# Kernel optimization log

Hardware: AMD Instinct MI355X
Metric: run time of the kernel (lower is better)

The kernel has to match this reference:

```python
import jax, jax.numpy as jnp
import numpy as np

B, DIM, H, W = 8, 512, 32, 32
HC, WC = 32, 32
NH, DH = 8, 64
DE = NH * DH  # dim_embed = 512


def setup_inputs() -> dict:
    key = jax.random.key(0)
    ks = jax.random.split(key, 6)
    return {
        "x": jax.random.normal(ks[0], (B, DIM, H, W), jnp.float32),
        "context": jax.random.normal(ks[1], (B, DIM, HC, WC), jnp.float32),
        "gamma": jnp.ones((DIM, 1, 1), jnp.float32),
        "w_q": jax.random.normal(ks[2], (DE, DIM), jnp.float32) * 0.02,
        "w_k": jax.random.normal(ks[3], (DE, DIM), jnp.float32) * 0.02,
        "w_v": jax.random.normal(ks[4], (DE, DIM), jnp.float32) * 0.02,
        "w_proj": jax.random.normal(ks[5], (DIM, DE), jnp.float32) * 0.02,
    }


def _rms_norm(t, gamma, scale):
    # torch F.normalize(dim=1): x / max(||x||_2, 1e-12) along channel axis
    nrm = jnp.sqrt(jnp.sum(t * t, axis=1, keepdims=True))
    return t / jnp.maximum(nrm, 1e-12) * scale * gamma


def _split_heads(t, h, w):
    # 'b (c n) h w -> (b n) (h w) c' with c=DH, n=NH
    b = t.shape[0]
    t = t.reshape(b, DH, NH, h, w).transpose(0, 2, 3, 4, 1)  # b n h w c
    return t.reshape(b * NH, h * w, DH)


def reference(x, context, gamma, w_q, w_k, w_v, w_proj):
    scale = float(DIM) ** 0.5
    xn = _rms_norm(x, gamma, scale)
    # faithful to source bug: self.norm (not norm_context) applied to context
    cn = _rms_norm(context, gamma, scale)

    q = jnp.einsum('bchw,oc->bohw', xn, w_q)
    k = jnp.einsum('bchw,oc->bohw', cn, w_k)
    v = jnp.einsum('bchw,oc->bohw', cn, w_v)

    q = _split_heads(q, H, W)      # (B*NH, H*W, DH)
    k = _split_heads(k, HC, WC)    # (B*NH, HC*WC, DH)
    v = _split_heads(v, HC, WC)

    qk = jnp.einsum('bmc,bnc->bmn', q, k) * (float(DH) ** -0.5)
    attn = jnp.einsum('bmn,bnc->bmc', jax.nn.softmax(qk, axis=-1) + 1e-8, v) + 1e-8

    # '(b n) (h w) c -> b (c n) h w'
    attn = attn.reshape(B, NH, H, W, DH).transpose(0, 4, 1, 2, 3).reshape(B, DE, H, W)
    return jnp.einsum('bchw,oc->bohw', attn, w_proj)
```

## Files before the change

kernel.cpp:

```cpp
#include <hip/hip_runtime.h>
#include <hip/hip_bf16.h>


typedef _Float16 half8v __attribute__((ext_vector_type(8)));
typedef __attribute__((ext_vector_type(4))) float float4v;

__device__ inline ushort f2h(float f) {
  union { _Float16 h; ushort u; } cv;
  cv.h = (_Float16)f;
  return cv.u;
}

__device__ inline void stage16(const void* g, void* l) {
  __builtin_amdgcn_global_load_lds(
      (const __attribute__((address_space(1))) unsigned*)g,
      (__attribute__((address_space(3))) unsigned*)l, 16, 0, 0);
}

__global__ __launch_bounds__(256) void tq_kernel(
    const float* __restrict__ x, const float* __restrict__ ctx,
    ushort* __restrict__ xT, ushort* __restrict__ cT,
    float* __restrict__ sx, float* __restrict__ sc) {
  const int tensor = blockIdx.z;
  const int b = blockIdx.y;
  const int pos0 = blockIdx.x << 5;
  const float* src = tensor ? ctx : x;
  ushort* dstT = tensor ? cT : xT;
  float* dstS = tensor ? sc : sx;
  const int t = threadIdx.x;

  __shared__ ushort tile[32 * 512];
  __shared__ float part[32][32];
  unsigned* tile32 = (unsigned*)tile;

  const int pcq = t & 7;
  const int crg = t >> 3;
  float ssq[4] = {0.f, 0.f, 0.f, 0.f};

  const float* srcb = src + ((size_t)b * 512) * 1024 + pos0;
  for (int p = 0; p < 8; ++p) {
    const int cr0 = p * 64 + crg * 2;
    float4 v0 = *(const float4*)&srcb[(size_t)cr0 * 1024 + pcq * 4];
    float4 v1 = *(const float4*)&srcb[(size_t)(cr0 + 1) * 1024 + pcq * 4];
    ssq[0] += v0.x * v0.x + v1.x * v1.x;
    ssq[1] += v0.y * v0.y + v1.y * v1.y;
    ssq[2] += v0.z * v0.z + v1.z * v1.z;
    ssq[3] += v0.w * v0.w + v1.w * v1.w;
    const int cp = cr0 >> 1;
    float e0[4] = {v0.x, v0.y, v0.z, v0.w};
    float e1[4] = {v1.x, v1.y, v1.z, v1.w};
#pragma unroll
    for (int j = 0; j < 4; ++j) {
      const int posl = pcq * 4 + j;
      unsigned pk = (unsigned)f2h(e0[j]) | ((unsigned)f2h(e1[j]) << 16);
      tile32[posl * 256 + (cp ^ posl)] = pk;
    }
  }
#pragma unroll
  for (int j = 0; j < 4; ++j) part[crg][pcq * 4 + j] = ssq[j];
  __syncthreads();
  if (t < 32) {
    float s = 0.f;
#pragma unroll
    for (int g2 = 0; g2 < 32; ++g2) s += part[g2][t];
    dstS[b * 1024 + pos0 + t] = 22.627416997969522f / fmaxf(sqrtf(s), 1e-12f);
  }
  ushort* ob = dstT + ((size_t)b * 1024 + pos0) * 512;
#pragma unroll
  for (int ii = 0; ii < 8; ++ii) {
    const int m = t + ii * 256;
    const int posl = m >> 6, c16 = m & 63;
    uint4 u;
    u.x = tile32[posl * 256 + ((c16 * 4 + 0) ^ posl)];
    u.y = tile32[posl * 256 + ((c16 * 4 + 1) ^ posl)];
    u.z = tile32[posl * 256 + ((c16 * 4 + 2) ^ posl)];
    u.w = tile32[posl * 256 + ((c16 * 4 + 3) ^ posl)];
    *(uint4*)&ob[(size_t)posl * 512 + c16 * 8] = u;
  }
}

__global__ __launch_bounds__(256) void wconv_kernel(
    const float* __restrict__ wq, const float* __restrict__ wk,
    const float* __restrict__ wv, const float* __restrict__ wp,
    const float* __restrict__ gamma, ushort* __restrict__ wf) {
  const int m = blockIdx.y;
  const float* W = (m == 0) ? wq : (m == 1) ? wk : (m == 2) ? wv : wp;
  const int r = blockIdx.x * 4 + (threadIdx.x >> 6);
  const int c8 = (threadIdx.x & 63) * 8;
  ushort h[8];
  if (m < 3) {
    const int o = ((r & 63) << 3) + (r >> 6);
    const float* wr_ = &W[(size_t)o * 512 + c8];
#pragma unroll
    for (int j = 0; j < 8; ++j) h[j] = f2h(wr_[j] * gamma[c8 + j]);
  } else {
#pragma unroll
    for (int j = 0; j < 8; ++j) {
      const int cc = c8 + j;
      const int cs = ((cc & 63) << 3) + (cc >> 6);
      h[j] = f2h(W[(size_t)r * 512 + cs]);
    }
  }
  ushort* dst = &wf[((size_t)m * 512 + r) * 512 + c8];
  uint4 u;
  u.x = (unsigned)h[0] | ((unsigned)h[1] << 16);
  u.y = (unsigned)h[2] | ((unsigned)h[3] << 16);
  u.z = (unsigned)h[4] | ((unsigned)h[5] << 16);
  u.w = (unsigned)h[6] | ((unsigned)h[7] << 16);
  *(uint4*)dst = u;
}

__global__ __launch_bounds__(256, 2) void qkv_kernel(
    const ushort* __restrict__ xT, const ushort* __restrict__ cT,
    const ushort* __restrict__ wf, const float* __restrict__ sx,
    const float* __restrict__ sc, ushort* __restrict__ qh,
    ushort* __restrict__ kh, ushort* __restrict__ vt) {
  const int z = blockIdx.z;
  const int proj = z % 3;
  const int b = z / 3;
  const ushort* XT = (proj == 0) ? xT : cT;
  const float* S = (proj == 0) ? sx : sc;
  const ushort* WF = wf + (size_t)proj * 262144;
  const int pos0 = blockIdx.x << 7;
  const int o0 = blockIdx.y << 7;

  __shared__ __align__(16) unsigned char lds[65536];
  unsigned char* Al = lds;
  unsigned char* Bl = lds + 32768;

  const int t = threadIdx.x, w = t >> 6, lane = t & 63;
  const int g = lane >> 4, l15 = lane & 15;
  const int wr = w >> 1, wc = w & 1;
  const int srow_ = lane >> 3;
  const int sslot16 = ((lane & 7) ^ srow_) << 4;

  const unsigned char* Asrc =
      (const unsigned char*)(XT + ((size_t)b * 1024 + pos0) * 512);
  const unsigned char* Bsrc = (const unsigned char*)(WF + (size_t)o0 * 512);

#define QSTAGE(buf, kk)                                                     \
  do {                                                                      \
    _Pragma("unroll") for (int i = 0; i < 4; ++i) {                         \
      const int j = (w << 2) + i;                                           \
      stage16(Asrc + (size_t)((j << 3) + srow_) * 1024 + (kk)*128 + sslot16,\
              Al + (buf)*16384 + (j << 10));                                \
      stage16(Bsrc + (size_t)((j << 3) + srow_) * 1024 + (kk)*128 + sslot16,\
              Bl + (buf)*16384 + (j << 10));                                \
    }                                                                       \
  } while (0)

  float4v acc[4][4];
#pragma unroll
  for (int i = 0; i < 4; ++i)
#pragma unroll
    for (int j2 = 0; j2 < 4; ++j2) acc[i][j2] = (float4v){0.f, 0.f, 0.f, 0.f};

  QSTAGE(0, 0);
  __syncthreads();

  for (int kk = 0; kk < 8; ++kk) {
    const int cur = kk & 1;
    if (kk < 7) QSTAGE(cur ^ 1, kk + 1);
    const unsigned char* At = Al + cur * 16384;
    const unsigned char* Bt = Bl + cur * 16384;
    half8v af[4][2], bf[4][2];
#pragma unroll
    for (int mt = 0; mt < 4; ++mt) {
      const int row = (wr << 6) + (mt << 4) + l15;
      const unsigned char* rb = At + row * 128;
      af[mt][0] = *(const half8v*)(rb + (((g) ^ (row & 7)) << 4));
      af[mt][1] = *(const half8v*)(rb + (((4 + g) ^ (row & 7)) << 4));
    }
#pragma unroll
    for (int nt = 0; nt < 4; ++nt) {
      const int row = (wc << 6) + (nt << 4) + l15;
      const unsigned char* rb = Bt + row * 128;
      bf[nt][0] = *(const half8v*)(rb + (((g) ^ (row & 7)) << 4));
      bf[nt][1] = *(const half8v*)(rb + (((4 + g) ^ (row & 7)) << 4));
    }
    if (proj < 2) {
#pragma unroll
      for (int mt = 0; mt < 4; ++mt)
#pragma unroll
        for (int nt = 0; nt < 4; ++nt) {
          acc[mt][nt] = __builtin_amdgcn_mfma_f32_16x16x32_f16(
              af[mt][0], bf[nt][0], acc[mt][nt], 0, 0, 0);
          acc[mt][nt] = __builtin_amdgcn_mfma_f32_16x16x32_f16(
              af[mt][1], bf[nt][1], acc[mt][nt], 0, 0, 0);
        }
    } else {
#pragma unroll
      for (int mt = 0; mt < 4; ++mt)
#pragma unroll
        for (int nt = 0; nt < 4; ++nt) {
          acc[mt][nt] = __builtin_amdgcn_mfma_f32_16x16x32_f16(
              bf[nt][0], af[mt][0], acc[mt][nt], 0, 0, 0);
          acc[mt][nt] = __builtin_amdgcn_mfma_f32_16x16x32_f16(
              bf[nt][1], af[mt][1], acc[mt][nt], 0, 0, 0);
        }
    }
    __syncthreads();
  }
#undef QSTAGE

  if (proj < 2) {
    ushort* Out = (proj == 0) ? qh : kh;
#pragma unroll
    for (int mt = 0; mt < 4; ++mt) {
      const int posb = pos0 + (wr << 6) + (mt << 4) + (g << 2);
      float4 sv = *(const float4*)&S[b * 1024 + posb];
      float sarr[4] = {sv.x, sv.y, sv.z, sv.w};
#pragma unroll
      for (int nt = 0; nt < 4; ++nt) {
        const int oo = o0 + (wc << 6) + (nt << 4) + l15;
#pragma unroll
        for (int r = 0; r < 3 + 1; ++r) {
          float val = acc[mt][nt][r] * sarr[r];
          Out[((size_t)(b * 1024 + posb + r)) * 512 + oo] = f2h(val);
        }
      }
    }
  } else {
#pragma unroll
    for (int mt = 0; mt < 4; ++mt) {
      const int pos = pos0 + (wr << 6) + (mt << 4) + l15;
      const float sval = S[b * 1024 + pos];
#pragma unroll
      for (int nt = 0; nt < 4; ++nt) {
        const int ob = o0 + (wc << 6) + (nt << 4) + (g << 2);
#pragma unroll
        for (int r = 0; r < 4; ++r) {
          const int oo = ob + r;
          vt[((size_t)(b * 512 + oo)) * 1024 + pos] = f2h(acc[mt][nt][r] * sval);
        }
      }
    }
  }
}

__global__ __launch_bounds__(512, 2) void attn_kernel(
    const ushort* __restrict__ qh, const ushort* __restrict__ kh,
    const ushort* __restrict__ vt, ushort* __restrict__ am) {
  __shared__ __align__(16) unsigned char lds[65536];

  const int bh = blockIdx.y;
  const int b = bh >> 3, n = bh & 7;
  const int mbase = blockIdx.x << 8;
  const int t = threadIdx.x;
  const int w = t >> 6;
  const int lane = t & 63;
  const int g = lane >> 4;
  const int l15 = lane & 15;
  const int swz = (l15 & 7) << 4;

  half8v qf[2][2];
#pragma unroll
  for (int qt = 0; qt < 2; ++qt) {
    const size_t qrow = (size_t)b * 1024 + mbase + w * 32 + qt * 16 + l15;
#pragma unroll
    for (int c = 0; c < 2; ++c)
      qf[qt][c] = *(const half8v*)(qh + qrow * 512 + n * 64 + c * 32 + g * 8);
  }

  float4v o[2][4];
#pragma unroll
  for (int qt = 0; qt < 2; ++qt)
#pragma unroll
    for (int dt = 0; dt < 4; ++dt) o[qt][dt] = (float4v){0.f, 0.f, 0.f, 0.f};
  float rsum[2] = {0.f, 0.f};

  const int srow = (w << 3) + (lane >> 3);
  const int scol = ((lane & 7) ^ (lane >> 3)) << 4;
  const unsigned char* kgb =
      (const unsigned char*)(kh + (size_t)b * 524288 + n * 64) + srow * 1024 +
      scol;
  const unsigned char* vgb =
      (const unsigned char*)(vt + (size_t)(b * 8 + n) * 65536) + srow * 2048 +
      scol;
  unsigned char* Kl = lds;
  unsigned char* Vl = lds + 16384;
  unsigned char* Pl = lds + 32768 + w * 4096;

#define ASTAGE(buf, kt)                                            \
  do {                                                             \
    stage16(kgb + (size_t)(kt)*65536, Kl + (buf)*8192 + w * 1024); \
    stage16(vgb + (size_t)(kt)*128, Vl + (buf)*8192 + w * 1024);   \
  } while (0)

  ASTAGE(0, 0);
  __syncthreads();

  for (int kt = 0; kt < 16; ++kt) {
    const int cur = kt & 1;
    if (kt < 15) ASTAGE(cur ^ 1, kt + 1);

    const unsigned char* Kc = Kl + cur * 8192;
    const unsigned char* Vc = Vl + cur * 8192;

    float4v st[4][2];
#pragma unroll
    for (int ktile = 0; ktile < 4; ++ktile) {
      const unsigned char* krow = Kc + (ktile * 16 + l15) * 128;
      half8v kf0 = *(const half8v*)(krow + ((g * 16) ^ swz));
      half8v kf1 = *(const half8v*)(krow + ((64 + g * 16) ^ swz));
#pragma unroll
      for (int qt = 0; qt < 2; ++qt) {
        float4v a2 = {0.f, 0.f, 0.f, 0.f};
        a2 = __builtin_amdgcn_mfma_f32_16x16x32_f16(kf0, qf[qt][0], a2, 0, 0, 0);
        a2 = __builtin_amdgcn_mfma_f32_16x16x32_f16(kf1, qf[qt][1], a2, 0, 0, 0);
        st[ktile][qt] = a2;
      }
    }

#pragma unroll
    for (int qt = 0; qt < 2; ++qt) {
      unsigned char* prowp = Pl + (qt * 16 + l15) * 128;
#pragma unroll
      for (int ktile = 0; ktile < 4; ++ktile) {
        union { unsigned long long u; ushort s[4]; } pk;
        float4v sv = st[ktile][qt];
#pragma unroll
        for (int r = 0; r < 4; ++r) {
          float p = __expf(sv[r] * 0.125f);
          rsum[qt] += p;
          pk.s[r] = f2h(p);
        }
        *(unsigned long long*)(prowp + ((ktile * 32 + g * 8) ^ swz)) = pk.u;
      }
    }

    half8v pf[2][2];
#pragma unroll
    for (int qt = 0; qt < 2; ++qt)
#pragma unroll
      for (int c = 0; c < 2; ++c)
        pf[qt][c] = *(const half8v*)(Pl + (qt * 16 + l15) * 128 +
                                     ((c * 64 + g * 16) ^ swz));
#pragma unroll
    for (int dt = 0; dt < 4; ++dt) {
      const unsigned char* vrow = Vc + (dt * 16 + l15) * 128;
      half8v vf0 = *(const half8v*)(vrow + ((g * 16) ^ swz));
      half8v vf1 = *(const half8v*)(vrow + ((64 + g * 16) ^ swz));
#pragma unroll
      for (int qt = 0; qt < 2; ++qt) {
        o[qt][dt] = __builtin_amdgcn_mfma_f32_16x16x32_f16(pf[qt][0], vf0,
                                                           o[qt][dt], 0, 0, 0);
        o[qt][dt] = __builtin_amdgcn_mfma_f32_16x16x32_f16(pf[qt][1], vf1,
                                                           o[qt][dt], 0, 0, 0);
      }
    }
    __syncthreads();
  }
#undef ASTAGE

#pragma unroll
  for (int qt = 0; qt < 2; ++qt) {
    float r = rsum[qt];
    r += __shfl_xor(r, 16, 64);
    r += __shfl_xor(r, 32, 64);
    rsum[qt] = 1.0f / r;
  }

#pragma unroll
  for (int qt = 0; qt < 2; ++qt) {
#pragma unroll
    for (int dt = 0; dt < 4; ++dt) {
      float4v ov = o[qt][dt];
      const int d = dt * 16 + l15;
#pragma unroll
      for (int r = 0; r < 4; ++r) {
        float inv = __shfl(rsum[qt], (lane & 48) | (g * 4 + r), 64);
        const int pos = mbase + w * 32 + qt * 16 + g * 4 + r;
        am[((size_t)(b * 1024 + pos)) * 512 + n * 64 + d] = f2h(ov[r] * inv);
      }
    }
  }
}

__global__ __launch_bounds__(256, 2) void proj_kernel(
    const ushort* __restrict__ am, const ushort* __restrict__ wf3,
    float* __restrict__ out) {
  const int b = blockIdx.z;
  const int pos0 = blockIdx.x << 7;
  const int o0 = blockIdx.y << 7;

  __shared__ __align__(16) unsigned char lds[65536];
  unsigned char* Al = lds;
  unsigned char* Bl = lds + 32768;

  const int t = threadIdx.x, w = t >> 6, lane = t & 63;
  const int g = lane >> 4, l15 = lane & 15;
  const int wr = w >> 1, wc = w & 1;
  const int srow_ = lane >> 3;
  const int sslot16 = ((lane & 7) ^ srow_) << 4;

  const unsigned char* Asrc = (const unsigned char*)(wf3 + (size_t)o0 * 512);
  const unsigned char* Bsrc =
      (const unsigned char*)(am + ((size_t)b * 1024 + pos0) * 512);

#define PSTAGE(buf, kk)                                                     \
  do {                                                                      \
    _Pragma("unroll") for (int i = 0; i < 4; ++i) {                         \
      const int j = (w << 2) + i;                                           \
      stage16(Asrc + (size_t)((j << 3) + srow_) * 1024 + (kk)*128 + sslot16,\
              Al + (buf)*16384 + (j << 10));                                \
      stage16(Bsrc + (size_t)((j << 3) + srow_) * 1024 + (kk)*128 + sslot16,\
              Bl + (buf)*16384 + (j << 10));                                \
    }                                                                       \
  } while (0)

  float4v acc[4][4];
#pragma unroll
  for (int i = 0; i < 4; ++i)
#pragma unroll
    for (int j2 = 0; j2 < 4; ++j2) acc[i][j2] = (float4v){0.f, 0.f, 0.f, 0.f};

  PSTAGE(0, 0);
  __syncthreads();

  for (int kk = 0; kk < 8; ++kk) {
    const int cur = kk & 1;
    if (kk < 7) PSTAGE(cur ^ 1, kk + 1);
    const unsigned char* At = Al + cur * 16384;
    const unsigned char* Bt = Bl + cur * 16384;
    half8v af[4][2], bf[4][2];
#pragma unroll
    for (int mt = 0; mt < 4; ++mt) {
      const int row = (wr << 6) + (mt << 4) + l15;
      const unsigned char* rb = At + row * 128;
      af[mt][0] = *(const half8v*)(rb + (((g) ^ (row & 7)) << 4));
      af[mt][1] = *(const half8v*)(rb + (((4 + g) ^ (row & 7)) << 4));
    }
#pragma unroll
    for (int nt = 0; nt < 4; ++nt) {
      const int row = (wc << 6) + (nt << 4) + l15;
      const unsigned char* rb = Bt + row * 128;
      bf[nt][0] = *(const half8v*)(rb + (((g) ^ (row & 7)) << 4));
      bf[nt][1] = *(const half8v*)(rb + (((4 + g) ^ (row & 7)) << 4));
    }
#pragma unroll
    for (int mt = 0; mt < 4; ++mt)
#pragma unroll
      for (int nt = 0; nt < 4; ++nt) {
        acc[mt][nt] = __builtin_amdgcn_mfma_f32_16x16x32_f16(
            af[mt][0], bf[nt][0], acc[mt][nt], 0, 0, 0);
        acc[mt][nt] = __builtin_amdgcn_mfma_f32_16x16x32_f16(
            af[mt][1], bf[nt][1], acc[mt][nt], 0, 0, 0);
      }
    __syncthreads();
  }
#undef PSTAGE

#pragma unroll
  for (int mt = 0; mt < 4; ++mt) {
    const int ob = o0 + (wr << 6) + (mt << 4) + (g << 2);
#pragma unroll
    for (int nt = 0; nt < 4; ++nt) {
      const int pos = pos0 + (wc << 6) + (nt << 4) + l15;
#pragma unroll
      for (int r = 0; r < 4; ++r) {
        out[((size_t)(b * 512 + ob + r)) * 1024 + pos] = acc[mt][nt][r];
      }
    }
  }
}

extern "C" void kernel_launch(void* const* d_in, const int* in_sizes, int n_in,
                              void* d_out, int out_size, void* d_ws,
                              size_t ws_size, hipStream_t stream) {
  const float* x = (const float*)d_in[0];
  const float* ctx = (const float*)d_in[1];
  const float* gamma = (const float*)d_in[2];
  const float* wq = (const float*)d_in[3];
  const float* wk = (const float*)d_in[4];
  const float* wv = (const float*)d_in[5];
  const float* wp = (const float*)d_in[6];
  float* out = (float*)d_out;

  char* ws = (char*)d_ws;
  float* sx = (float*)(ws);
  float* sc = (float*)(ws + 32768);
  ushort* xT = (ushort*)(ws + 65536);
  ushort* cT = (ushort*)(ws + 65536 + 8388608);
  ushort* wf = (ushort*)(ws + 65536 + 16777216);
  ushort* qh = (ushort*)(ws + 65536 + 18874368);
  ushort* kh = (ushort*)(ws + 65536 + 27262976);
  ushort* vt = (ushort*)(ws + 65536 + 35651584);
  ushort* am = xT;

  tq_kernel<<<dim3(32, 8, 2), 256, 0, stream>>>(x, ctx, xT, cT, sx, sc);
  wconv_kernel<<<dim3(128, 4), 256, 0, stream>>>(wq, wk, wv, wp, gamma, wf);
  qkv_kernel<<<dim3(8, 4, 24), 256, 0, stream>>>(xT, cT, wf, sx, sc, qh, kh,
                                                 vt);
  attn_kernel<<<dim3(4, 64), 512, 0, stream>>>(qh, kh, vt, am);
  proj_kernel<<<dim3(8, 4, 8), 256, 0, stream>>>(am, wf + 3 * 262144, out);
}
```

Before: 68.69 us.

## Merge prep kernels, retile QKV GEMM to 256x256 with phased pipeline, fold softmax scale

Merges the transpose/normalize kernel and the weight conversion kernel into one launch. Rewrites the QKV GEMM to 512-thread blocks with 256x256 tiles in 128KB LDS, driven by a hand-scheduled double-buffered pipeline using explicit barriers, waitcnt and setprio. The 1/sqrt(DH) scale moves into the Q epilogue and V is stored with vectorized writes. Softmax exp packing switches to cvt_pkrtz, which changes the fp16 rounding mode to round-toward-zero.

```diff
diff --git a/kernel.cpp b/kernel.cpp
--- a/kernel.cpp
+++ b/kernel.cpp
@@ -3,6 +3,7 @@
 
 
 typedef _Float16 half8v __attribute__((ext_vector_type(8)));
+typedef __fp16 fp16x2 __attribute__((ext_vector_type(2)));
 typedef __attribute__((ext_vector_type(4))) float float4v;
 
 __device__ inline ushort f2h(float f) {
@@ -17,222 +18,280 @@
       (__attribute__((address_space(3))) unsigned*)l, 16, 0, 0);
 }
 
-__global__ __launch_bounds__(256) void tq_kernel(
+__global__ __launch_bounds__(256) void prep_kernel(
     const float* __restrict__ x, const float* __restrict__ ctx,
-    ushort* __restrict__ xT, ushort* __restrict__ cT,
-    float* __restrict__ sx, float* __restrict__ sc) {
-  const int tensor = blockIdx.z;
-  const int b = blockIdx.y;
-  const int pos0 = blockIdx.x << 5;
-  const float* src = tensor ? ctx : x;
-  ushort* dstT = tensor ? cT : xT;
-  float* dstS = tensor ? sc : sx;
-  const int t = threadIdx.x;
-
+    const float* __restrict__ wq, const float* __restrict__ wk,
+    const float* __restrict__ wv, const float* __restrict__ wp,
+    const float* __restrict__ gamma, ushort* __restrict__ xT,
+    ushort* __restrict__ cT, float* __restrict__ sx, float* __restrict__ sc,
+    ushort* __restrict__ wf) {
   __shared__ ushort tile[32 * 512];
   __shared__ float part[32][32];
-  unsigned* tile32 = (unsigned*)tile;
-
-  const int pcq = t & 7;
-  const int crg = t >> 3;
-  float ssq[4] = {0.f, 0.f, 0.f, 0.f};
-
-  const float* srcb = src + ((size_t)b * 512) * 1024 + pos0;
-  for (int p = 0; p < 8; ++p) {
-    const int cr0 = p * 64 + crg * 2;
-    float4 v0 = *(const float4*)&srcb[(size_t)cr0 * 1024 + pcq * 4];
-    float4 v1 = *(const float4*)&srcb[(size_t)(cr0 + 1) * 1024 + pcq * 4];
-    ssq[0] += v0.x * v0.x + v1.x * v1.x;
-    ssq[1] += v0.y * v0.y + v1.y * v1.y;
-    ssq[2] += v0.z * v0.z + v1.z * v1.z;
-    ssq[3] += v0.w * v0.w + v1.w * v1.w;
-    const int cp = cr0 >> 1;
-    float e0[4] = {v0.x, v0.y, v0.z, v0.w};
-    float e1[4] = {v1.x, v1.y, v1.z, v1.w};
-#pragma unroll
-    for (int j = 0; j < 4; ++j) {
-      const int posl = pcq * 4 + j;
-      unsigned pk = (unsigned)f2h(e0[j]) | ((unsigned)f2h(e1[j]) << 16);
-      tile32[posl * 256 + (cp ^ posl)] = pk;
-    }
-  }
-#pragma unroll
-  for (int j = 0; j < 4; ++j) part[crg][pcq * 4 + j] = ssq[j];
-  __syncthreads();
-  if (t < 32) {
-    float s = 0.f;
-#pragma unroll
-    for (int g2 = 0; g2 < 32; ++g2) s += part[g2][t];
-    dstS[b * 1024 + pos0 + t] = 22.627416997969522f / fmaxf(sqrtf(s), 1e-12f);
-  }
-  ushort* ob = dstT + ((size_t)b * 1024 + pos0) * 512;
-#pragma unroll
-  for (int ii = 0; ii < 8; ++ii) {
-    const int m = t + ii * 256;
-    const int posl = m >> 6, c16 = m & 63;
+  const int bid = blockIdx.x;
+  const int t = threadIdx.x;
+
+  if (bid < 512) {
+    const int tensor = bid >> 8;
+    const int b = (bid >> 5) & 7;
+    const int pos0 = (bid & 31) << 5;
+    const float* src = tensor ? ctx : x;
+    ushort* dstT = tensor ? cT : xT;
+    float* dstS = tensor ? sc : sx;
+    unsigned* tile32 = (unsigned*)tile;
+
+    const int pcq = t & 7;
+    const int crg = t >> 3;
+    float ssq[4] = {0.f, 0.f, 0.f, 0.f};
+
+    const float* srcb = src + ((size_t)b * 512) * 1024 + pos0;
+    for (int p = 0; p < 8; ++p) {
+      const int cr0 = p * 64 + crg * 2;
+      float4 v0 = *(const float4*)&srcb[(size_t)cr0 * 1024 + pcq * 4];
+      float4 v1 = *(const float4*)&srcb[(size_t)(cr0 + 1) * 1024 + pcq * 4];
+      ssq[0] += v0.x * v0.x + v1.x * v1.x;
+      ssq[1] += v0.y * v0.y + v1.y * v1.y;
+      ssq[2] += v0.z * v0.z + v1.z * v1.z;
+      ssq[3] += v0.w * v0.w + v1.w * v1.w;
+      const int cp = cr0 >> 1;
+      float e0[4] = {v0.x, v0.y, v0.z, v0.w};
+      float e1[4] = {v1.x, v1.y, v1.z, v1.w};
+#pragma unroll
+      for (int j = 0; j < 4; ++j) {
+        const int posl = pcq * 4 + j;
+        unsigned pk = (unsigned)f2h(e0[j]) | ((unsigned)f2h(e1[j]) << 16);
+        tile32[posl * 256 + (cp ^ posl)] = pk;
+      }
+    }
+#pragma unroll
+    for (int j = 0; j < 4; ++j) part[crg][pcq * 4 + j] = ssq[j];
+    __syncthreads();
+    if (t < 32) {
+      float s = 0.f;
+#pragma unroll
+      for (int g2 = 0; g2 < 32; ++g2) s += part[g2][t];
+      dstS[b * 1024 + pos0 + t] =
+          22.627416997969522f / fmaxf(sqrtf(s), 1e-12f);
+    }
+    ushort* ob = dstT + ((size_t)b * 1024 + pos0) * 512;
+#pragma unroll
+    for (int ii = 0; ii < 8; ++ii) {
+      const int m = t + ii * 256;
+      const int posl = m >> 6, c16 = m & 63;
+      uint4 u;
+      u.x = tile32[posl * 256 + ((c16 * 4 + 0) ^ posl)];
+      u.y = tile32[posl * 256 + ((c16 * 4 + 1) ^ posl)];
+      u.z = tile32[posl * 256 + ((c16 * 4 + 2) ^ posl)];
+      u.w = tile32[posl * 256 + ((c16 * 4 + 3) ^ posl)];
+      *(uint4*)&ob[(size_t)posl * 512 + c16 * 8] = u;
+    }
+  } else {
+    const int wbid = bid - 512;
+    const int m = wbid >> 7;
+    const float* W = (m == 0) ? wq : (m == 1) ? wk : (m == 2) ? wv : wp;
+    const int r = (wbid & 127) * 4 + (t >> 6);
+    const int c8 = (t & 63) * 8;
+    ushort h[8];
+    if (m < 3) {
+      const int o = ((r & 63) << 3) + (r >> 6);
+      const float* wr_ = &W[(size_t)o * 512 + c8];
+#pragma unroll
+      for (int j = 0; j < 8; ++j) h[j] = f2h(wr_[j] * gamma[c8 + j]);
+    } else {
+#pragma unroll
+      for (int j = 0; j < 8; ++j) {
+        const int cc = c8 + j;
+        const int cs = ((cc & 63) << 3) + (cc >> 6);
+        h[j] = f2h(W[(size_t)r * 512 + cs]);
+      }
+    }
+    ushort* dst = &wf[((size_t)m * 512 + r) * 512 + c8];
     uint4 u;
-    u.x = tile32[posl * 256 + ((c16 * 4 + 0) ^ posl)];
-    u.y = tile32[posl * 256 + ((c16 * 4 + 1) ^ posl)];
-    u.z = tile32[posl * 256 + ((c16 * 4 + 2) ^ posl)];
-    u.w = tile32[posl * 256 + ((c16 * 4 + 3) ^ posl)];
-    *(uint4*)&ob[(size_t)posl * 512 + c16 * 8] = u;
-  }
-}
-
-__global__ __launch_bounds__(256) void wconv_kernel(
-    const float* __restrict__ wq, const float* __restrict__ wk,
-    const float* __restrict__ wv, const float* __restrict__ wp,
-    const float* __restrict__ gamma, ushort* __restrict__ wf) {
-  const int m = blockIdx.y;
-  const float* W = (m == 0) ? wq : (m == 1) ? wk : (m == 2) ? wv : wp;
-  const int r = blockIdx.x * 4 + (threadIdx.x >> 6);
-  const int c8 = (threadIdx.x & 63) * 8;
-  ushort h[8];
-  if (m < 3) {
-    const int o = ((r & 63) << 3) + (r >> 6);
-    const float* wr_ = &W[(size_t)o * 512 + c8];
-#pragma unroll
-    for (int j = 0; j < 8; ++j) h[j] = f2h(wr_[j] * gamma[c8 + j]);
-  } else {
-#pragma unroll
-    for (int j = 0; j < 8; ++j) {
-      const int cc = c8 + j;
-      const int cs = ((cc & 63) << 3) + (cc >> 6);
-      h[j] = f2h(W[(size_t)r * 512 + cs]);
-    }
-  }
-  ushort* dst = &wf[((size_t)m * 512 + r) * 512 + c8];
-  uint4 u;
-  u.x = (unsigned)h[0] | ((unsigned)h[1] << 16);
-  u.y = (unsigned)h[2] | ((unsigned)h[3] << 16);
-  u.z = (unsigned)h[4] | ((unsigned)h[5] << 16);
-  u.w = (unsigned)h[6] | ((unsigned)h[7] << 16);
-  *(uint4*)dst = u;
-}
-
-__global__ __launch_bounds__(256, 2) void qkv_kernel(
+    u.x = (unsigned)h[0] | ((unsigned)h[1] << 16);
+    u.y = (unsigned)h[2] | ((unsigned)h[3] << 16);
+    u.z = (unsigned)h[4] | ((unsigned)h[5] << 16);
+    u.w = (unsigned)h[6] | ((unsigned)h[7] << 16);
+    *(uint4*)dst = u;
+  }
+}
+
+__global__ __launch_bounds__(512, 2) void qkv_kernel(
     const ushort* __restrict__ xT, const ushort* __restrict__ cT,
     const ushort* __restrict__ wf, const float* __restrict__ sx,
     const float* __restrict__ sc, ushort* __restrict__ qh,
     ushort* __restrict__ kh, ushort* __restrict__ vt) {
-  const int z = blockIdx.z;
-  const int proj = z % 3;
-  const int b = z / 3;
+  __shared__ __align__(16) unsigned char lds[131072];
+  const int proj = blockIdx.y >> 1;
+  const int b = blockIdx.z;
+  const int pos0 = blockIdx.x << 8;
+  const int o0g = blockIdx.y << 8;
+
+  const int t = threadIdx.x;
+  const int w = t >> 6, lane = t & 63;
+  const int wr = w >> 2, wc = w & 3;
+  const int g = lane >> 4, l15 = lane & 15;
+
   const ushort* XT = (proj == 0) ? xT : cT;
+  const unsigned char* Ag =
+      (const unsigned char*)XT + ((size_t)(b * 1024 + pos0) << 10);
+  const unsigned char* Bg = (const unsigned char*)wf + ((size_t)o0g << 10);
+
+  const int srw = t >> 3;
+  const int srcslot16 = ((t & 7) ^ (srw & 7)) << 4;
+  unsigned char* Albase = lds;
+  unsigned char* Blbase = lds + 65536;
+
+#define UNIT(gbase, lbase, d, h, kt)                                    \
+  do {                                                                  \
+    const unsigned char* _s = (gbase) +                                 \
+        (((size_t)((h)*128 + srw)) << 10) + ((kt) << 7) + srcslot16;    \
+    unsigned char* _l = (lbase) + (d)*32768 + (h)*16384 + t * 16;       \
+    stage16(_s, _l);                                                    \
+    stage16(_s + (64 << 10), _l + 8192);                                \
+  } while (0)
+
+#define PHASE(q)                                                        \
+  do {                                                                  \
+    asm volatile("" ::: "memory");                                      \
+    __builtin_amdgcn_s_barrier();                                       \
+    asm volatile("s_waitcnt lgkmcnt(0)" ::: "memory");                  \
+    __builtin_amdgcn_sched_barrier(0);                                  \
+    __builtin_amdgcn_s_setprio(1);                                      \
+    _Pragma("unroll") for (int ii = 0; ii < 2; ++ii)                    \
+        _Pragma("unroll") for (int nf = 0; nf < 4; ++nf) {              \
+      acc[(q)*2 + ii][nf] = __builtin_amdgcn_mfma_f32_16x16x32_f16(     \
+          af[ii][0], bf[nf][0], acc[(q)*2 + ii][nf], 0, 0, 0);          \
+      acc[(q)*2 + ii][nf] = __builtin_amdgcn_mfma_f32_16x16x32_f16(     \
+          af[ii][1], bf[nf][1], acc[(q)*2 + ii][nf], 0, 0, 0);          \
+    }                                                                   \
+    __builtin_amdgcn_s_setprio(0);                                      \
+  } while (0)
+
+#define TRAIL()                                                         \
+  do {                                                                  \
+    asm volatile("" ::: "memory");                                      \
+    __builtin_amdgcn_s_barrier();                                       \
+    asm volatile("" ::: "memory");                                      \
+  } while (0)
+
+#define LDA(d, mtb)                                                     \
+  _Pragma("unroll") for (int ii = 0; ii < 2; ++ii) {                    \
+    const unsigned char* _r =                                           \
+        Albase + (d)*32768 + aoff + ((mtb) + ii) * 2048;                \
+    af[ii][0] = *(const half8v*)(_r + sl0);                             \
+    af[ii][1] = *(const half8v*)(_r + sl1);                             \
+  }
+
+#define LDB(d)                                                          \
+  _Pragma("unroll") for (int nf = 0; nf < 4; ++nf) {                    \
+    const unsigned char* _r = Blbase + (d)*32768 + boff + nf * 2048;    \
+    bf[nf][0] = *(const half8v*)(_r + sl0);                             \
+    bf[nf][1] = *(const half8v*)(_r + sl1);                             \
+  }
+
+  const int sl0 = ((g ^ (l15 & 7)) << 4);
+  const int sl1 = (((4 + g) ^ (l15 & 7)) << 4);
+  const int aoff = (wr << 14) + (l15 << 7);
+  const int boff = ((wc >> 1) << 14) + ((((wc & 1) << 6) + l15) << 7);
+
+  float4v acc[8][4];
+#pragma unroll
+  for (int i = 0; i < 8; ++i)
+#pragma unroll
+    for (int j = 0; j < 4; ++j) acc[i][j] = (float4v){0.f, 0.f, 0.f, 0.f};
+
+  UNIT(Ag, Albase, 0, 0, 0);
+  UNIT(Ag, Albase, 0, 1, 0);
+  UNIT(Bg, Blbase, 0, 0, 0);
+  UNIT(Bg, Blbase, 0, 1, 0);
+  UNIT(Bg, Blbase, 1, 0, 1);
+  UNIT(Bg, Blbase, 1, 1, 1);
+  asm volatile("s_waitcnt vmcnt(4)" ::: "memory");
+  TRAIL();
+
+  for (int i = 0; i < 4; ++i) {
+    const int t0 = 2 * i;
+    const bool st = (i < 3);
+    half8v af[2][2], bf[4][2];
+
+    LDB(0); LDA(0, 0);
+    UNIT(Ag, Albase, 1, 0, t0 + 1);
+    PHASE(0); TRAIL();
+
+    LDA(0, 2);
+    UNIT(Ag, Albase, 1, 1, t0 + 1);
+    PHASE(1); TRAIL();
+
+    LDA(0, 4);
+    if (st) UNIT(Bg, Blbase, 0, 0, t0 + 2);
+    PHASE(2); TRAIL();
+
+    LDA(0, 6);
+    if (st) UNIT(Bg, Blbase, 0, 1, t0 + 2);
+    PHASE(3);
+    if (st) {
+      asm volatile("s_waitcnt vmcnt(4)" ::: "memory");
+    } else {
+      asm volatile("s_waitcnt vmcnt(0)" ::: "memory");
+    }
+    TRAIL();
+
+    LDB(1); LDA(1, 0);
+    if (st) UNIT(Ag, Albase, 0, 0, t0 + 2);
+    PHASE(0); TRAIL();
+
+    LDA(1, 2);
+    if (st) UNIT(Ag, Albase, 0, 1, t0 + 2);
+    PHASE(1); TRAIL();
+
+    LDA(1, 4);
+    if (st) UNIT(Bg, Blbase, 1, 0, t0 + 3);
+    PHASE(2); TRAIL();
+
+    LDA(1, 6);
+    if (st) UNIT(Bg, Blbase, 1, 1, t0 + 3);
+    PHASE(3);
+    if (st) asm volatile("s_waitcnt vmcnt(4)" ::: "memory");
+    TRAIL();
+  }
+#undef UNIT
+#undef PHASE
+#undef TRAIL
+#undef LDA
+#undef LDB
+
   const float* S = (proj == 0) ? sx : sc;
-  const ushort* WF = wf + (size_t)proj * 262144;
-  const int pos0 = blockIdx.x << 7;
-  const int o0 = blockIdx.y << 7;
-
-  __shared__ __align__(16) unsigned char lds[65536];
-  unsigned char* Al = lds;
-  unsigned char* Bl = lds + 32768;
-
-  const int t = threadIdx.x, w = t >> 6, lane = t & 63;
-  const int g = lane >> 4, l15 = lane & 15;
-  const int wr = w >> 1, wc = w & 1;
-  const int srow_ = lane >> 3;
-  const int sslot16 = ((lane & 7) ^ srow_) << 4;
-
-  const unsigned char* Asrc =
-      (const unsigned char*)(XT + ((size_t)b * 1024 + pos0) * 512);
-  const unsigned char* Bsrc = (const unsigned char*)(WF + (size_t)o0 * 512);
-
-#define QSTAGE(buf, kk)                                                     \
-  do {                                                                      \
-    _Pragma("unroll") for (int i = 0; i < 4; ++i) {                         \
-      const int j = (w << 2) + i;                                           \
-      stage16(Asrc + (size_t)((j << 3) + srow_) * 1024 + (kk)*128 + sslot16,\
-              Al + (buf)*16384 + (j << 10));                                \
-      stage16(Bsrc + (size_t)((j << 3) + srow_) * 1024 + (kk)*128 + sslot16,\
-              Bl + (buf)*16384 + (j << 10));                                \
-    }                                                                       \
-  } while (0)
-
-  float4v acc[4][4];
-#pragma unroll
-  for (int i = 0; i < 4; ++i)
-#pragma unroll
-    for (int j2 = 0; j2 < 4; ++j2) acc[i][j2] = (float4v){0.f, 0.f, 0.f, 0.f};
-
-  QSTAGE(0, 0);
-  __syncthreads();
-
-  for (int kk = 0; kk < 8; ++kk) {
-    const int cur = kk & 1;
-    if (kk < 7) QSTAGE(cur ^ 1, kk + 1);
-    const unsigned char* At = Al + cur * 16384;
-    const unsigned char* Bt = Bl + cur * 16384;
-    half8v af[4][2], bf[4][2];
-#pragma unroll
-    for (int mt = 0; mt < 4; ++mt) {
-      const int row = (wr << 6) + (mt << 4) + l15;
-      const unsigned char* rb = At + row * 128;
-      af[mt][0] = *(const half8v*)(rb + (((g) ^ (row & 7)) << 4));
-      af[mt][1] = *(const half8v*)(rb + (((4 + g) ^ (row & 7)) << 4));
-    }
-#pragma unroll
-    for (int nt = 0; nt < 4; ++nt) {
-      const int row = (wc << 6) + (nt << 4) + l15;
-      const unsigned char* rb = Bt + row * 128;
-      bf[nt][0] = *(const half8v*)(rb + (((g) ^ (row & 7)) << 4));
-      bf[nt][1] = *(const half8v*)(rb + (((4 + g) ^ (row & 7)) << 4));
-    }
-    if (proj < 2) {
-#pragma unroll
-      for (int mt = 0; mt < 4; ++mt)
-#pragma unroll
-        for (int nt = 0; nt < 4; ++nt) {
-          acc[mt][nt] = __builtin_amdgcn_mfma_f32_16x16x32_f16(
-              af[mt][0], bf[nt][0], acc[mt][nt], 0, 0, 0);
-          acc[mt][nt] = __builtin_amdgcn_mfma_f32_16x16x32_f16(
-              af[mt][1], bf[nt][1], acc[mt][nt], 0, 0, 0);
-        }
-    } else {
-#pragma unroll
-      for (int mt = 0; mt < 4; ++mt)
-#pragma unroll
-        for (int nt = 0; nt < 4; ++nt) {
-          acc[mt][nt] = __builtin_amdgcn_mfma_f32_16x16x32_f16(
-              bf[nt][0], af[mt][0], acc[mt][nt], 0, 0, 0);
-          acc[mt][nt] = __builtin_amdgcn_mfma_f32_16x16x32_f16(
-              bf[nt][1], af[mt][1], acc[mt][nt], 0, 0, 0);
-        }
-    }
-    __syncthreads();
-  }
-#undef QSTAGE
-
+  const float qsc = (proj == 0) ? 0.125f : 1.0f;
+  const int o_in = (o0g & 511) + (wc << 6);
   if (proj < 2) {
     ushort* Out = (proj == 0) ? qh : kh;
 #pragma unroll
-    for (int mt = 0; mt < 4; ++mt) {
-      const int posb = pos0 + (wr << 6) + (mt << 4) + (g << 2);
+    for (int mt = 0; mt < 8; ++mt) {
+      const int posb = pos0 + (wr << 7) + (mt << 4) + (g << 2);
       float4 sv = *(const float4*)&S[b * 1024 + posb];
-      float sarr[4] = {sv.x, sv.y, sv.z, sv.w};
-#pragma unroll
-      for (int nt = 0; nt < 4; ++nt) {
-        const int oo = o0 + (wc << 6) + (nt << 4) + l15;
-#pragma unroll
-        for (int r = 0; r < 3 + 1; ++r) {
-          float val = acc[mt][nt][r] * sarr[r];
-          Out[((size_t)(b * 1024 + posb + r)) * 512 + oo] = f2h(val);
-        }
+      float sa[4] = {sv.x * qsc, sv.y * qsc, sv.z * qsc, sv.w * qsc};
+#pragma unroll
+      for (int nf = 0; nf < 4; ++nf) {
+        const int oo = o_in + (nf << 4) + l15;
+        ushort* op = Out + ((size_t)(b * 1024 + posb)) * 512 + oo;
+#pragma unroll
+        for (int r = 0; r < 4; ++r)
+          op[(size_t)r * 512] = f2h(acc[mt][nf][r] * sa[r]);
       }
     }
   } else {
 #pragma unroll
-    for (int mt = 0; mt < 4; ++mt) {
-      const int pos = pos0 + (wr << 6) + (mt << 4) + l15;
-      const float sval = S[b * 1024 + pos];
-#pragma unroll
-      for (int nt = 0; nt < 4; ++nt) {
-        const int ob = o0 + (wc << 6) + (nt << 4) + (g << 2);
-#pragma unroll
-        for (int r = 0; r < 4; ++r) {
-          const int oo = ob + r;
-          vt[((size_t)(b * 512 + oo)) * 1024 + pos] = f2h(acc[mt][nt][r] * sval);
-        }
+    for (int mt = 0; mt < 8; ++mt) {
+      const int posb = pos0 + (wr << 7) + (mt << 4) + (g << 2);
+      float4 sv = *(const float4*)&S[b * 1024 + posb];
+#pragma unroll
+      for (int nf = 0; nf < 4; ++nf) {
+        const int oo = o_in + (nf << 4) + l15;
+        ushort4 h4;
+        h4.x = f2h(acc[mt][nf][0] * sv.x);
+        h4.y = f2h(acc[mt][nf][1] * sv.y);
+        h4.z = f2h(acc[mt][nf][2] * sv.z);
+        h4.w = f2h(acc[mt][nf][3] * sv.w);
+        *(ushort4*)(vt + ((size_t)(b * 512 + oo)) * 1024 + posb) = h4;
       }
     }
   }
@@ -317,15 +376,15 @@
       unsigned char* prowp = Pl + (qt * 16 + l15) * 128;
 #pragma unroll
       for (int ktile = 0; ktile < 4; ++ktile) {
-        union { unsigned long long u; ushort s[4]; } pk;
         float4v sv = st[ktile][qt];
-#pragma unroll
-        for (int r = 0; r < 4; ++r) {
-          float p = __expf(sv[r] * 0.125f);
-          rsum[qt] += p;
-          pk.s[r] = f2h(p);
-        }
-        *(unsigned long long*)(prowp + ((ktile * 32 + g * 8) ^ swz)) = pk.u;
+        float p0 = __expf(sv[0]), p1 = __expf(sv[1]);
+        float p2 = __expf(sv[2]), p3 = __expf(sv[3]);
+        rsum[qt] += (p0 + p1) + (p2 + p3);
+        union { fp16x2 h; unsigned u; } ua, ub;
+        ua.h = __builtin_amdgcn_cvt_pkrtz(p0, p1);
+        ub.h = __builtin_amdgcn_cvt_pkrtz(p2, p3);
+        unsigned long long pu = ((unsigned long long)ub.u << 32) | ua.u;
+        *(unsigned long long*)(prowp + ((ktile * 32 + g * 8) ^ swz)) = pu;
       }
     }
 
@@ -488,10 +547,10 @@
   ushort* vt = (ushort*)(ws + 65536 + 35651584);
   ushort* am = xT;
 
-  tq_kernel<<<dim3(32, 8, 2), 256, 0, stream>>>(x, ctx, xT, cT, sx, sc);
-  wconv_kernel<<<dim3(128, 4), 256, 0, stream>>>(wq, wk, wv, wp, gamma, wf);
-  qkv_kernel<<<dim3(8, 4, 24), 256, 0, stream>>>(xT, cT, wf, sx, sc, qh, kh,
-                                                 vt);
+  prep_kernel<<<1024, 256, 0, stream>>>(x, ctx, wq, wk, wv, wp, gamma, xT, cT,
+                                        sx, sc, wf);
+  qkv_kernel<<<dim3(4, 6, 8), 512, 0, stream>>>(xT, cT, wf, sx, sc, qh, kh,
+                                                vt);
   attn_kernel<<<dim3(4, 64), 512, 0, stream>>>(qh, kh, vt, am);
   proj_kernel<<<dim3(8, 4, 8), 256, 0, stream>>>(am, wf + 3 * 262144, out);
 }
```

Measured after the change: 69.92 us. Within noise of the previous version (+1.8%).
